# Optimization experiments

Measured on AMD Instinct MI355X. Metric: run time of the kernel, lower is better.

Reference implementation:

```python
import jax, jax.numpy as jnp
import numpy as np

NEG_INF = -1e30

def setup_inputs() -> dict:
    key = jax.random.key(0)
    k1, k2, k3 = jax.random.split(key, 3)
    B, H, S, D = 2, 16, 2048, 128
    q = jax.random.normal(k1, (B, H, S, D), dtype=jnp.float32)
    k = jax.random.normal(k2, (B, H, S, D), dtype=jnp.float32)
    v = jax.random.normal(k3, (B, H, S, D), dtype=jnp.float32)
    return {"q": q, "k": k, "v": v}

def reference(q, k, v):
    # F.scaled_dot_product_attention(q, k, v, is_causal=True), MATH backend:
    # full score matrix, causal mask (top-left aligned: j <= i), softmax, bmm.
    D = q.shape[-1]
    scale = 1.0 / jnp.sqrt(jnp.asarray(D, dtype=q.dtype))
    scores = jnp.einsum('bhqd,bhkd->bhqk', q, k) * scale  # [B,H,S,S]
    Sq, Sk = scores.shape[-2], scores.shape[-1]
    causal = jnp.arange(Sk)[None, :] <= jnp.arange(Sq)[:, None]  # [Sq,Sk]
    scores = jnp.where(causal[None, None], scores, NEG_INF)
    attn = jax.nn.softmax(scores, axis=-1)
    return jnp.einsum('bhqk,bhkd->bhqd', attn, v)
```

## Files before the change

### kernel.cpp

```cpp
#include <hip/hip_runtime.h>
#include <cstdint>
#include <cstddef>

typedef __attribute__((ext_vector_type(8))) short short8;
typedef __attribute__((ext_vector_type(4))) float floatx4;
typedef __attribute__((ext_vector_type(2))) unsigned int uint2v;

namespace {
constexpr int kBH  = 32;
constexpr int kS   = 2048;
constexpr int kD   = 128;
constexpr int kBQ  = 64;
constexpr int kBK  = 64;
constexpr int kNQT = kS / kBQ;
constexpr int PST  = 72;
constexpr size_t kKVElems = (size_t)kBH * kS * kD;
}

__device__ __forceinline__ unsigned short f32_bf16(float f) {
    union { float f; unsigned u; } c; c.f = f;
    unsigned u = c.u;
    u += 0x7FFFu + ((u >> 16) & 1u);
    return (unsigned short)(u >> 16);
}

__device__ __forceinline__ unsigned cvt_pk_bf16(float lo, float hi) {
    unsigned r;
    asm("v_cvt_pk_bf16_f32 %0, %1, %2" : "=v"(r) : "v"(lo), "v"(hi));
    return r;
}

__device__ __forceinline__ unsigned pack_bf16x2(float lo, float hi) {
    return cvt_pk_bf16(lo, hi);
}

__device__ __forceinline__ float fast_exp2(float x) {
#if __has_builtin(__builtin_amdgcn_exp2f)
    return __builtin_amdgcn_exp2f(x);
#else
    return __expf(x * 0.6931471805599453f);
#endif
}

__device__ __forceinline__ void gl_lds16(const void* g, void* l) {
    __builtin_amdgcn_global_load_lds(
        (const __attribute__((address_space(1))) unsigned int*)g,
        (__attribute__((address_space(3))) unsigned int*)l, 16, 0, 0);
}

__global__ __launch_bounds__(256)
void prepass(const float* __restrict__ K, const float* __restrict__ V,
             unsigned short* __restrict__ Kb, unsigned short* __restrict__ Vt) {
    const int b = (int)blockIdx.x;
    const int t = (int)threadIdx.x;
    if (b < 4096) {
        const size_t i0 = ((size_t)b * 256 + t) * 8;
        floatx4 a = *(const floatx4*)(K + i0);
        floatx4 c = *(const floatx4*)(K + i0 + 4);
        union { unsigned u[4]; short8 v; } pk;
        pk.u[0] = cvt_pk_bf16(a[0], a[1]);
        pk.u[1] = cvt_pk_bf16(a[2], a[3]);
        pk.u[2] = cvt_pk_bf16(c[0], c[1]);
        pk.u[3] = cvt_pk_bf16(c[2], c[3]);
        *(short8*)(Kb + i0) = pk.v;
    } else {
        __shared__ float ldsT[64][68];
        const int vb = b - 4096;
        const int bh = vb >> 6;
        const int rem = vb & 63;
        const int s0 = (rem >> 1) * 64;
        const int d0 = (rem & 1) * 64;
        const float* vbase = V + ((size_t)bh * kS + s0) * kD + d0;
        const int sr = t >> 4, c4 = (t & 15) * 4;
#pragma unroll
        for (int p = 0; p < 4; ++p) {
            const int s = p * 16 + sr;
            *(floatx4*)&ldsT[s][c4] = *(const floatx4*)(vbase + (size_t)s * kD + c4);
        }
        __syncthreads();
        const int dr = t >> 2, sc = (t & 3) * 16;
        union { unsigned u[8]; short8 v[2]; } pk;
#pragma unroll
        for (int j = 0; j < 8; ++j)
            pk.u[j] = cvt_pk_bf16(ldsT[sc + 2 * j][dr], ldsT[sc + 2 * j + 1][dr]);
        unsigned short* out = Vt + ((size_t)(bh * kD + d0 + dr)) * kS + s0 + sc;
        *(short8*)out = pk.v[0];
        *(short8*)(out + 8) = pk.v[1];
    }
}


struct TileState {
    short8  qf[4];
    floatx4 oacc[8];
    float   lsum[4];
};

__device__ __forceinline__ void tile_step(
    TileState& ts, const unsigned short* kT, const unsigned short* vT,
    unsigned short* pw, int l16, int quad, int rowl, bool doMask)
{
    floatx4 sacc[4];
    __builtin_amdgcn_s_setprio(1);
#pragma unroll
    for (int nt = 0; nt < 4; ++nt) {
        floatx4 acc = (floatx4){0.f, 0.f, 0.f, 0.f};
#pragma unroll
        for (int ks = 0; ks < 4; ++ks) {
            short8 kf = *(const short8*)&kT[(nt * 16 + l16) * 128 + (((ks * 4 + quad) ^ l16) << 3)];
            acc = __builtin_amdgcn_mfma_f32_16x16x32_bf16(ts.qf[ks], kf, acc, 0, 0, 0);
        }
        sacc[nt] = acc;
    }
    __builtin_amdgcn_s_setprio(0);

    if (doMask) {
#pragma unroll
        for (int nt = 0; nt < 4; ++nt) {
            const int col = nt * 16 + l16;
#pragma unroll
            for (int r = 0; r < 4; ++r)
                if (col > rowl + r) sacc[nt][r] = -1e30f;
        }
    }

#pragma unroll
    for (int nt = 0; nt < 4; ++nt)
#pragma unroll
        for (int r = 0; r < 4; ++r)
            sacc[nt][r] = fast_exp2(sacc[nt][r]);
#pragma unroll
    for (int r = 0; r < 4; ++r)
        ts.lsum[r] += (sacc[0][r] + sacc[1][r]) + (sacc[2][r] + sacc[3][r]);

#pragma unroll
    for (int r = 0; r < 4; ++r) {
#pragma unroll
        for (int np = 0; np < 2; ++np) {
            const unsigned u = cvt_pk_bf16(sacc[np * 2][r], sacc[np * 2 + 1][r]);
            pw[(quad * 4 + r) * PST + (np * 2) * 16 + l16]     = (unsigned short)u;
            pw[(quad * 4 + r) * PST + (np * 2 + 1) * 16 + l16] = (unsigned short)(u >> 16);
        }
    }

    short8 pf[2];
#pragma unroll
    for (int ks = 0; ks < 2; ++ks)
        pf[ks] = *(const short8*)&pw[l16 * PST + ks * 32 + quad * 8];

    __builtin_amdgcn_s_setprio(1);
#pragma unroll
    for (int nd = 0; nd < 8; ++nd) {
        floatx4 acc = ts.oacc[nd];
#pragma unroll
        for (int ks = 0; ks < 2; ++ks) {
            short8 vf = *(const short8*)&vT[(nd * 16 + l16) * 64 + ((((ks * 4 + quad)) ^ (l16 & 7)) << 3)];
            acc = __builtin_amdgcn_mfma_f32_16x16x32_bf16(pf[ks], vf, acc, 0, 0, 0);
        }
        ts.oacc[nd] = acc;
    }
    __builtin_amdgcn_s_setprio(0);
}

__device__ __forceinline__ void tile_step_dual(
    TileState& A, TileState& B, const unsigned short* kT, const unsigned short* vT,
    unsigned short* pw, int l16, int quad, int rowl, bool maskA)
{
    floatx4 saccA[4], saccB[4];
    __builtin_amdgcn_s_setprio(1);
#pragma unroll
    for (int nt = 0; nt < 4; ++nt) {
        floatx4 accA = (floatx4){0.f, 0.f, 0.f, 0.f};
        floatx4 accB = (floatx4){0.f, 0.f, 0.f, 0.f};
#pragma unroll
        for (int ks = 0; ks < 4; ++ks) {
            short8 kf = *(const short8*)&kT[(nt * 16 + l16) * 128 + (((ks * 4 + quad) ^ l16) << 3)];
            accA = __builtin_amdgcn_mfma_f32_16x16x32_bf16(A.qf[ks], kf, accA, 0, 0, 0);
            accB = __builtin_amdgcn_mfma_f32_16x16x32_bf16(B.qf[ks], kf, accB, 0, 0, 0);
        }
        saccA[nt] = accA;
        saccB[nt] = accB;
    }
    __builtin_amdgcn_s_setprio(0);

    if (maskA) {
#pragma unroll
        for (int nt = 0; nt < 4; ++nt) {
            const int col = nt * 16 + l16;
#pragma unroll
            for (int r = 0; r < 4; ++r)
                if (col > rowl + r) saccA[nt][r] = -1e30f;
        }
    }

#pragma unroll
    for (int nt = 0; nt < 4; ++nt)
#pragma unroll
        for (int r = 0; r < 4; ++r) {
            saccA[nt][r] = fast_exp2(saccA[nt][r]);
            saccB[nt][r] = fast_exp2(saccB[nt][r]);
        }
#pragma unroll
    for (int r = 0; r < 4; ++r) {
        A.lsum[r] += (saccA[0][r] + saccA[1][r]) + (saccA[2][r] + saccA[3][r]);
        B.lsum[r] += (saccB[0][r] + saccB[1][r]) + (saccB[2][r] + saccB[3][r]);
    }

    short8 pfA[2], pfB[2];
#pragma unroll
    for (int r = 0; r < 4; ++r)
#pragma unroll
        for (int np = 0; np < 2; ++np) {
            const unsigned u = cvt_pk_bf16(saccA[np * 2][r], saccA[np * 2 + 1][r]);
            pw[(quad * 4 + r) * PST + (np * 2) * 16 + l16]     = (unsigned short)u;
            pw[(quad * 4 + r) * PST + (np * 2 + 1) * 16 + l16] = (unsigned short)(u >> 16);
        }
#pragma unroll
    for (int ks = 0; ks < 2; ++ks)
        pfA[ks] = *(const short8*)&pw[l16 * PST + ks * 32 + quad * 8];
#pragma unroll
    for (int r = 0; r < 4; ++r)
#pragma unroll
        for (int np = 0; np < 2; ++np) {
            const unsigned u = cvt_pk_bf16(saccB[np * 2][r], saccB[np * 2 + 1][r]);
            pw[(quad * 4 + r) * PST + (np * 2) * 16 + l16]     = (unsigned short)u;
            pw[(quad * 4 + r) * PST + (np * 2 + 1) * 16 + l16] = (unsigned short)(u >> 16);
        }
#pragma unroll
    for (int ks = 0; ks < 2; ++ks)
        pfB[ks] = *(const short8*)&pw[l16 * PST + ks * 32 + quad * 8];

    __builtin_amdgcn_s_setprio(1);
#pragma unroll
    for (int nd = 0; nd < 8; ++nd) {
        floatx4 accA = A.oacc[nd];
        floatx4 accB = B.oacc[nd];
#pragma unroll
        for (int ks = 0; ks < 2; ++ks) {
            short8 vf = *(const short8*)&vT[(nd * 16 + l16) * 64 + ((((ks * 4 + quad)) ^ (l16 & 7)) << 3)];
            accA = __builtin_amdgcn_mfma_f32_16x16x32_bf16(pfA[ks], vf, accA, 0, 0, 0);
            accB = __builtin_amdgcn_mfma_f32_16x16x32_bf16(pfB[ks], vf, accB, 0, 0, 0);
        }
        A.oacc[nd] = accA;
        B.oacc[nd] = accB;
    }
    __builtin_amdgcn_s_setprio(0);
}

__global__ __launch_bounds__(256, 2)
void fa_fwd_ws(const float* __restrict__ Qg, const unsigned short* __restrict__ Kb,
               const unsigned short* __restrict__ Vt, float* __restrict__ Og) {
    const int id = (int)blockIdx.x;
    const int qA = id >> 5;
    const int qB = kNQT - 1 - qA;
    const int bh = id & (kBH - 1);
    const int t    = (int)threadIdx.x;
    const int wave = t >> 6;
    const int lane = t & 63;
    const int quad = lane >> 4;
    const int l16  = lane & 15;
    const int rowl = wave * 16 + quad * 4;

    __shared__ __align__(16) unsigned short kT0[kBK * 128];
    __shared__ __align__(16) unsigned short kT1[kBK * 128];
    __shared__ __align__(16) unsigned short vT0[kD * 64];
    __shared__ __align__(16) unsigned short vT1[kD * 64];
    __shared__ __align__(16) unsigned short pT[4 * 16 * PST];
    unsigned short* pw = &pT[wave * 16 * PST];

    const float scale = 0.12751744459649126f;

    TileState A, B;
#pragma unroll
    for (int i = 0; i < 8; ++i) { A.oacc[i] = (floatx4){0,0,0,0}; B.oacc[i] = (floatx4){0,0,0,0}; }
#pragma unroll
    for (int r = 0; r < 4; ++r) { A.lsum[r] = 0.f; B.lsum[r] = 0.f; }

    {
        const float* qpA = Qg + ((size_t)bh * kS + qA * kBQ + wave * 16 + l16) * kD;
        const float* qpB = Qg + ((size_t)bh * kS + qB * kBQ + wave * 16 + l16) * kD;
#pragma unroll
        for (int ks = 0; ks < 4; ++ks) {
            const int d0 = ks * 32 + quad * 8;
            floatx4 a0 = *(const floatx4*)(qpA + d0);
            floatx4 a1 = *(const floatx4*)(qpA + d0 + 4);
            floatx4 b0 = *(const floatx4*)(qpB + d0);
            floatx4 b1 = *(const floatx4*)(qpB + d0 + 4);
            union { unsigned u[4]; short8 v; } pa, pb;
            pa.u[0] = cvt_pk_bf16(a0[0] * scale, a0[1] * scale);
            pa.u[1] = cvt_pk_bf16(a0[2] * scale, a0[3] * scale);
            pa.u[2] = cvt_pk_bf16(a1[0] * scale, a1[1] * scale);
            pa.u[3] = cvt_pk_bf16(a1[2] * scale, a1[3] * scale);
            pb.u[0] = cvt_pk_bf16(b0[0] * scale, b0[1] * scale);
            pb.u[1] = cvt_pk_bf16(b0[2] * scale, b0[3] * scale);
            pb.u[2] = cvt_pk_bf16(b1[0] * scale, b1[1] * scale);
            pb.u[3] = cvt_pk_bf16(b1[2] * scale, b1[3] * scale);
            A.qf[ks] = pa.v;
            B.qf[ks] = pb.v;
        }
    }

    const unsigned short* kBase = Kb + (size_t)bh * kS * kD;
    const unsigned short* vBase = Vt + (size_t)bh * kD * kS;

    auto stage = [&](int kt, unsigned short* kDst, unsigned short* vDst) {
        const int kj0 = kt * kBK;
        const int rbase = wave * 16;
#pragma unroll
        for (int i = 0; i < 4; ++i) {
            const int row = rbase + i * 4 + (lane >> 4);
            const int cg  = (lane & 15) ^ (row & 15);
            gl_lds16(kBase + ((size_t)(kj0 + row)) * kD + cg * 8,
                     &kDst[(rbase + i * 4) * 128]);
        }
        const int dbase = wave * 32;
#pragma unroll
        for (int i = 0; i < 4; ++i) {
            const int d  = dbase + i * 8 + (lane >> 3);
            const int cg = (lane & 7) ^ (d & 7);
            gl_lds16(vBase + (size_t)d * kS + kj0 + cg * 8,
                     &vDst[(dbase + i * 8) * 64]);
        }
    };

    const int last = qB;
    stage(0, kT0, vT0);
    __syncthreads();

    int kt = 0;
    for (;;) {
        if (kt < last) stage(kt + 1, kT1, vT1);
        if (kt <= qA) tile_step_dual(A, B, kT0, vT0, pw, l16, quad, rowl, kt == qA);
        else          tile_step(B, kT0, vT0, pw, l16, quad, rowl, kt == last);
        __syncthreads();
        if (kt == last) break;
        ++kt;
        if (kt < last) stage(kt + 1, kT0, vT0);
        if (kt <= qA) tile_step_dual(A, B, kT1, vT1, pw, l16, quad, rowl, kt == qA);
        else          tile_step(B, kT1, vT1, pw, l16, quad, rowl, kt == last);
        __syncthreads();
        if (kt == last) break;
        ++kt;
    }

#pragma unroll
    for (int tile = 0; tile < 2; ++tile) {
        TileState& ts = tile ? B : A;
        const int qt = tile ? qB : qA;
        float ls[4];
#pragma unroll
        for (int r = 0; r < 4; ++r) ls[r] = ts.lsum[r];
#pragma unroll
        for (int off = 1; off < 16; off <<= 1)
#pragma unroll
            for (int r = 0; r < 4; ++r)
                ls[r] += __shfl_xor(ls[r], off, 64);
        float inv[4];
#pragma unroll
        for (int r = 0; r < 4; ++r) inv[r] = 1.0f / ls[r];
        float* ob = Og + ((size_t)bh * kS + qt * kBQ + wave * 16 + quad * 4) * kD;
#pragma unroll
        for (int nd = 0; nd < 8; ++nd)
#pragma unroll
            for (int r = 0; r < 4; ++r)
                ob[(size_t)r * kD + nd * 16 + l16] = ts.oacc[nd][r] * inv[r];
    }
}

namespace {
constexpr int KSTf = 136;
constexpr int VSTf = 72;
}

__device__ __forceinline__ void tile_step_f(
    TileState& ts, const unsigned short* kT, const unsigned short* vT,
    unsigned short* pw, int l16, int quad, int rowl, bool doMask)
{
    floatx4 sacc[4];
    __builtin_amdgcn_s_setprio(1);
#pragma unroll
    for (int nt = 0; nt < 4; ++nt) {
        floatx4 acc = (floatx4){0.f, 0.f, 0.f, 0.f};
#pragma unroll
        for (int ks = 0; ks < 4; ++ks) {
            short8 kf = *(const short8*)&kT[(nt * 16 + l16) * KSTf + ks * 32 + quad * 8];
            acc = __builtin_amdgcn_mfma_f32_16x16x32_bf16(ts.qf[ks], kf, acc, 0, 0, 0);
        }
        sacc[nt] = acc;
    }
    __builtin_amdgcn_s_setprio(0);
    if (doMask) {
#pragma unroll
        for (int nt = 0; nt < 4; ++nt) {
            const int col = nt * 16 + l16;
#pragma unroll
            for (int r = 0; r < 4; ++r)
                if (col > rowl + r) sacc[nt][r] = -1e30f;
        }
    }
#pragma unroll
    for (int nt = 0; nt < 4; ++nt)
#pragma unroll
        for (int r = 0; r < 4; ++r)
            sacc[nt][r] = fast_exp2(sacc[nt][r]);
#pragma unroll
    for (int r = 0; r < 4; ++r)
        ts.lsum[r] += (sacc[0][r] + sacc[1][r]) + (sacc[2][r] + sacc[3][r]);
#pragma unroll
    for (int r = 0; r < 4; ++r) {
#pragma unroll
        for (int np = 0; np < 2; ++np) {
            const unsigned u = cvt_pk_bf16(sacc[np * 2][r], sacc[np * 2 + 1][r]);
            pw[(quad * 4 + r) * PST + (np * 2) * 16 + l16]     = (unsigned short)u;
            pw[(quad * 4 + r) * PST + (np * 2 + 1) * 16 + l16] = (unsigned short)(u >> 16);
        }
    }
    short8 pf[2];
#pragma unroll
    for (int ks = 0; ks < 2; ++ks)
        pf[ks] = *(const short8*)&pw[l16 * PST + ks * 32 + quad * 8];
    __builtin_amdgcn_s_setprio(1);
#pragma unroll
    for (int nd = 0; nd < 8; ++nd) {
        floatx4 acc = ts.oacc[nd];
#pragma unroll
        for (int ks = 0; ks < 2; ++ks) {
            short8 vf = *(const short8*)&vT[(nd * 16 + l16) * VSTf + ks * 32 + quad * 8];
            acc = __builtin_amdgcn_mfma_f32_16x16x32_bf16(pf[ks], vf, acc, 0, 0, 0);
        }
        ts.oacc[nd] = acc;
    }
    __builtin_amdgcn_s_setprio(0);
}

__global__ __launch_bounds__(256, 2)
void fa_fwd_fallback(const float* __restrict__ Qg, const float* __restrict__ Kg,
                     const float* __restrict__ Vg, float* __restrict__ Og) {
    const int id = (int)blockIdx.x;
    const int qA = id >> 5;
    const int qB = kNQT - 1 - qA;
    const int bh = id & (kBH - 1);
    const int t    = (int)threadIdx.x;
    const int wave = t >> 6;
    const int lane = t & 63;
    const int quad = lane >> 4;
    const int l16  = lane & 15;
    const int rowl = wave * 16 + quad * 4;

    __shared__ __align__(16) unsigned short kT[2][kBK * KSTf];
    __shared__ __align__(16) unsigned short vT[2][kD * VSTf];
    __shared__ __align__(16) unsigned short pT[4 * 16 * PST];
    unsigned short* pw = &pT[wave * 16 * PST];

    const float scale = 0.12751744459649126f;

    TileState A, B;
#pragma unroll
    for (int i = 0; i < 8; ++i) { A.oacc[i] = (floatx4){0,0,0,0}; B.oacc[i] = (floatx4){0,0,0,0}; }
#pragma unroll
    for (int r = 0; r < 4; ++r) { A.lsum[r] = 0.f; B.lsum[r] = 0.f; }
    {
        const float* qpA = Qg + ((size_t)bh * kS + qA * kBQ + wave * 16 + l16) * kD;
        const float* qpB = Qg + ((size_t)bh * kS + qB * kBQ + wave * 16 + l16) * kD;
#pragma unroll
        for (int ks = 0; ks < 4; ++ks) {
            const int d0 = ks * 32 + quad * 8;
            floatx4 a0 = *(const floatx4*)(qpA + d0);
            floatx4 a1 = *(const floatx4*)(qpA + d0 + 4);
            floatx4 b0 = *(const floatx4*)(qpB + d0);
            floatx4 b1 = *(const floatx4*)(qpB + d0 + 4);
            union { unsigned u[4]; short8 v; } pa, pb;
            pa.u[0] = cvt_pk_bf16(a0[0] * scale, a0[1] * scale);
            pa.u[1] = cvt_pk_bf16(a0[2] * scale, a0[3] * scale);
            pa.u[2] = cvt_pk_bf16(a1[0] * scale, a1[1] * scale);
            pa.u[3] = cvt_pk_bf16(a1[2] * scale, a1[3] * scale);
            pb.u[0] = cvt_pk_bf16(b0[0] * scale, b0[1] * scale);
            pb.u[1] = cvt_pk_bf16(b0[2] * scale, b0[3] * scale);
            pb.u[2] = cvt_pk_bf16(b1[0] * scale, b1[1] * scale);
            pb.u[3] = cvt_pk_bf16(b1[2] * scale, b1[3] * scale);
            A.qf[ks] = pa.v;
            B.qf[ks] = pb.v;
        }
    }

    const int kRow8 = t >> 5;
    const int kCol4 = t & 31;
    const int vD    = t & 127;
    const int vR2   = t >> 7;
    const float* kBaseH = Kg + (size_t)bh * kS * kD;
    const float* vBaseH = Vg + (size_t)bh * kS * kD;
    floatx4 kpre[8];
    float   vpreL[16], vpreH[16];

    auto issue_kv_loads = [&](int kt) {
        const float* kb = kBaseH + (size_t)(kt * kBK) * kD;
        const float* vb = vBaseH + (size_t)(kt * kBK) * kD;
#pragma unroll
        for (int p = 0; p < 8; ++p)
            kpre[p] = *(const floatx4*)(kb + (size_t)(p * 8 + kRow8) * kD + kCol4 * 4);
#pragma unroll
        for (int p = 0; p < 16; ++p) {
            const int j = p * 2 + vR2;
            vpreL[p] = vb[(size_t)(2 * j) * kD + vD];
            vpreH[p] = vb[(size_t)(2 * j + 1) * kD + vD];
        }
    };
    auto store_kv = [&](int buf) {
#pragma unroll
        for (int p = 0; p < 8; ++p) {
            union { unsigned u[2]; uint2v v; } w;
            w.u[0] = cvt_pk_bf16(kpre[p][0], kpre[p][1]);
            w.u[1] = cvt_pk_bf16(kpre[p][2], kpre[p][3]);
            *(uint2v*)&kT[buf][(p * 8 + kRow8) * KSTf + kCol4 * 4] = w.v;
        }
#pragma unroll
        for (int p = 0; p < 16; ++p) {
            const int j = p * 2 + vR2;
            *(unsigned*)&vT[buf][vD * VSTf + 2 * j] = pack_bf16x2(vpreL[p], vpreH[p]);
        }
    };

    const int last = qB;
    issue_kv_loads(0);
    store_kv(0);
    __syncthreads();
    for (int kt = 0; kt <= last; ++kt) {
        const int buf = kt & 1;
        if (kt < last) issue_kv_loads(kt + 1);
        if (kt <= qA) tile_step_f(A, kT[buf], vT[buf], pw, l16, quad, rowl, kt == qA);
        tile_step_f(B, kT[buf], vT[buf], pw, l16, quad, rowl, kt == last);
        if (kt < last) {
            store_kv(buf ^ 1);
            __syncthreads();
        }
    }
#pragma unroll
    for (int tile = 0; tile < 2; ++tile) {
        TileState& ts = tile ? B : A;
        const int qt = tile ? qB : qA;
        float ls[4];
#pragma unroll
        for (int r = 0; r < 4; ++r) ls[r] = ts.lsum[r];
#pragma unroll
        for (int off = 1; off < 16; off <<= 1)
#pragma unroll
            for (int r = 0; r < 4; ++r)
                ls[r] += __shfl_xor(ls[r], off, 64);
        float inv[4];
#pragma unroll
        for (int r = 0; r < 4; ++r) inv[r] = 1.0f / ls[r];
        float* ob = Og + ((size_t)bh * kS + qt * kBQ + wave * 16 + quad * 4) * kD;
#pragma unroll
        for (int nd = 0; nd < 8; ++nd)
#pragma unroll
            for (int r = 0; r < 4; ++r)
                ob[(size_t)r * kD + nd * 16 + l16] = ts.oacc[nd][r] * inv[r];
    }
}

extern "C" void kernel_launch(void* const* d_in, const int* in_sizes, int n_in,
                              void* d_out, int out_size, void* d_ws, size_t ws_size,
                              hipStream_t stream) {
    (void)in_sizes; (void)n_in; (void)out_size;
    const float* q = (const float*)d_in[0];
    const float* k = (const float*)d_in[1];
    const float* v = (const float*)d_in[2];
    float* o = (float*)d_out;
    const size_t need = 2 * kKVElems * sizeof(unsigned short);
    if (ws_size >= need) {
        unsigned short* Kb = (unsigned short*)d_ws;
        unsigned short* Vt = Kb + kKVElems;
        prepass<<<dim3(4096 + 2048), 256, 0, stream>>>(k, v, Kb, Vt);
        fa_fwd_ws<<<dim3((kNQT / 2) * kBH), 256, 0, stream>>>(q, Kb, Vt, o);
    } else {
        fa_fwd_fallback<<<dim3((kNQT / 2) * kBH), 256, 0, stream>>>(q, k, v, o);
    }
}
```

Baseline: 176.2 us.

## Use 512-thread blocks sharing K/V tiles across two query-tile pairs, XCD-aware mapping

Each block now runs 8 waves in two groups, each group handling its own pair of causal query tiles (2a+g and 31-2a-g). Both groups share the same staged K/V LDS tiles, which halves K/V global loads per query tile. Block IDs are remapped so that all blocks of one batch-head land on the same XCD, to improve L2 locality. The cost is fewer blocks (256) at one block per CU, and some waves sit idle on the final tile, since the two groups need different numbers of key tiles.

```diff
diff --git a/kernel.cpp b/kernel.cpp
--- a/kernel.cpp
+++ b/kernel.cpp
@@ -247,25 +247,32 @@
     __builtin_amdgcn_s_setprio(0);
 }
 
-__global__ __launch_bounds__(256, 2)
+__global__ __launch_bounds__(512, 1)
 void fa_fwd_ws(const float* __restrict__ Qg, const unsigned short* __restrict__ Kb,
                const unsigned short* __restrict__ Vt, float* __restrict__ Og) {
-    const int id = (int)blockIdx.x;
-    const int qA = id >> 5;
-    const int qB = kNQT - 1 - qA;
-    const int bh = id & (kBH - 1);
+    const int id  = (int)blockIdx.x;
+    const int xcd = id & 7;
+    const int j   = id >> 3;
+    const int bh  = xcd * 4 + (j & 3);
+    const int a   = j >> 2;
     const int t    = (int)threadIdx.x;
     const int wave = t >> 6;
+    const int g    = wave >> 2;
+    const int wsub = wave & 3;
     const int lane = t & 63;
     const int quad = lane >> 4;
     const int l16  = lane & 15;
-    const int rowl = wave * 16 + quad * 4;
+    const int rowl = wsub * 16 + quad * 4;
+
+    const int qAw  = 2 * a + g;
+    const int qBw  = 31 - 2 * a - g;
+    const int last = 31 - 2 * a;
 
     __shared__ __align__(16) unsigned short kT0[kBK * 128];
     __shared__ __align__(16) unsigned short kT1[kBK * 128];
     __shared__ __align__(16) unsigned short vT0[kD * 64];
     __shared__ __align__(16) unsigned short vT1[kD * 64];
-    __shared__ __align__(16) unsigned short pT[4 * 16 * PST];
+    __shared__ __align__(16) unsigned short pT[8 * 16 * PST];
     unsigned short* pw = &pT[wave * 16 * PST];
 
     const float scale = 0.12751744459649126f;
@@ -277,8 +284,8 @@
     for (int r = 0; r < 4; ++r) { A.lsum[r] = 0.f; B.lsum[r] = 0.f; }
 
     {
-        const float* qpA = Qg + ((size_t)bh * kS + qA * kBQ + wave * 16 + l16) * kD;
-        const float* qpB = Qg + ((size_t)bh * kS + qB * kBQ + wave * 16 + l16) * kD;
+        const float* qpA = Qg + ((size_t)bh * kS + qAw * kBQ + wsub * 16 + l16) * kD;
+        const float* qpB = Qg + ((size_t)bh * kS + qBw * kBQ + wsub * 16 + l16) * kD;
 #pragma unroll
         for (int ks = 0; ks < 4; ++ks) {
             const int d0 = ks * 32 + quad * 8;
@@ -305,17 +312,17 @@
 
     auto stage = [&](int kt, unsigned short* kDst, unsigned short* vDst) {
         const int kj0 = kt * kBK;
-        const int rbase = wave * 16;
-#pragma unroll
-        for (int i = 0; i < 4; ++i) {
+        const int rbase = wave * 8;
+#pragma unroll
+        for (int i = 0; i < 2; ++i) {
             const int row = rbase + i * 4 + (lane >> 4);
             const int cg  = (lane & 15) ^ (row & 15);
             gl_lds16(kBase + ((size_t)(kj0 + row)) * kD + cg * 8,
                      &kDst[(rbase + i * 4) * 128]);
         }
-        const int dbase = wave * 32;
-#pragma unroll
-        for (int i = 0; i < 4; ++i) {
+        const int dbase = wave * 16;
+#pragma unroll
+        for (int i = 0; i < 2; ++i) {
             const int d  = dbase + i * 8 + (lane >> 3);
             const int cg = (lane & 7) ^ (d & 7);
             gl_lds16(vBase + (size_t)d * kS + kj0 + cg * 8,
@@ -323,21 +330,20 @@
         }
     };
 
-    const int last = qB;
     stage(0, kT0, vT0);
     __syncthreads();
 
     int kt = 0;
     for (;;) {
         if (kt < last) stage(kt + 1, kT1, vT1);
-        if (kt <= qA) tile_step_dual(A, B, kT0, vT0, pw, l16, quad, rowl, kt == qA);
-        else          tile_step(B, kT0, vT0, pw, l16, quad, rowl, kt == last);
+        if (kt <= qAw)      tile_step_dual(A, B, kT0, vT0, pw, l16, quad, rowl, kt == qAw);
+        else if (kt <= qBw) tile_step(B, kT0, vT0, pw, l16, quad, rowl, kt == qBw);
         __syncthreads();
         if (kt == last) break;
         ++kt;
         if (kt < last) stage(kt + 1, kT0, vT0);
-        if (kt <= qA) tile_step_dual(A, B, kT1, vT1, pw, l16, quad, rowl, kt == qA);
-        else          tile_step(B, kT1, vT1, pw, l16, quad, rowl, kt == last);
+        if (kt <= qAw)      tile_step_dual(A, B, kT1, vT1, pw, l16, quad, rowl, kt == qAw);
+        else if (kt <= qBw) tile_step(B, kT1, vT1, pw, l16, quad, rowl, kt == qBw);
         __syncthreads();
         if (kt == last) break;
         ++kt;
@@ -346,7 +352,7 @@
 #pragma unroll
     for (int tile = 0; tile < 2; ++tile) {
         TileState& ts = tile ? B : A;
-        const int qt = tile ? qB : qA;
+        const int qt = tile ? qBw : qAw;
         float ls[4];
 #pragma unroll
         for (int r = 0; r < 4; ++r) ls[r] = ts.lsum[r];
@@ -358,7 +364,7 @@
         float inv[4];
 #pragma unroll
         for (int r = 0; r < 4; ++r) inv[r] = 1.0f / ls[r];
-        float* ob = Og + ((size_t)bh * kS + qt * kBQ + wave * 16 + quad * 4) * kD;
+        float* ob = Og + ((size_t)bh * kS + qt * kBQ + wsub * 16 + quad * 4) * kD;
 #pragma unroll
         for (int nd = 0; nd < 8; ++nd)
 #pragma unroll
@@ -571,7 +577,7 @@
         unsigned short* Kb = (unsigned short*)d_ws;
         unsigned short* Vt = Kb + kKVElems;
         prepass<<<dim3(4096 + 2048), 256, 0, stream>>>(k, v, Kb, Vt);
-        fa_fwd_ws<<<dim3((kNQT / 2) * kBH), 256, 0, stream>>>(q, Kb, Vt, o);
+        fa_fwd_ws<<<dim3(256), 512, 0, stream>>>(q, Kb, Vt, o);
     } else {
         fa_fwd_fallback<<<dim3((kNQT / 2) * kBH), 256, 0, stream>>>(q, k, v, o);
     }
```

Result: no change. 175.5 us (-0.4%).
